# Performance work log

Measured on AMD Instinct MI355X. Metric: run time of the kernel, lower is better.

The kernel has to match this reference:

```python
import jax, jax.numpy as jnp
from jax import lax
import numpy as np

B, S, T = 1024, 512, 48


def setup_inputs() -> dict:
    key = jax.random.key(0)
    k1, k2, k3, k4, k5, k6 = jax.random.split(key, 6)
    emissions = jax.random.normal(k1, (B, S, T), dtype=jnp.float32)
    tags = jax.random.randint(k2, (B, S), 0, T, dtype=jnp.int32)
    # variable-length mask; length >= 1 so position 0 is always valid
    lengths = jax.random.randint(k3, (B,), 1, S + 1, dtype=jnp.int32)
    mask = (jnp.arange(S)[None, :] < lengths[:, None]).astype(jnp.float32)
    transitions = jax.random.normal(k4, (T, T), dtype=jnp.float32)
    start_transitions = jax.random.normal(k5, (T,), dtype=jnp.float32)
    end_transitions = jax.random.normal(k6, (T,), dtype=jnp.float32)
    return {
        "emissions": emissions,
        "tags": tags,
        "mask": mask,
        "transitions": transitions,
        "start_transitions": start_transitions,
        "end_transitions": end_transitions,
    }


def _gold_score(emissions, tags, mask, transitions, start_transitions, end_transitions):
    # score of the gold tag sequence (vectorized over time)
    score = start_transitions[tags[:, 0]]
    score = score + jnp.take_along_axis(emissions[:, 0], tags[:, 0:1], axis=1)[:, 0]
    # NOTE: original code indexes transitions[cur_tag, prev_tag] here (faithful)
    trans_sc = transitions[tags[:, 1:], tags[:, :-1]]                      # [B, S-1]
    emit_sc = jnp.take_along_axis(emissions[:, 1:], tags[:, 1:, None], axis=2)[..., 0]
    score = score + jnp.sum((trans_sc + emit_sc) * mask[:, 1:], axis=1)
    seq_last = mask.sum(axis=1).astype(jnp.int32) - 1                      # [B]
    last_tags = jnp.take_along_axis(tags, seq_last[:, None], axis=1)[:, 0]
    return score + end_transitions[last_tags]


def _forward_algorithm(emissions, mask, transitions, start_transitions, end_transitions):
    # log-partition via logsumexp recurrence, lax.scan over time
    init = start_transitions[None, :] + emissions[:, 0]                    # [B, T]

    def step(score, xs):
        em_i, m_i = xs                                                     # [B,T], [B]
        # next[b, cur] = logsumexp_prev(score[b,prev] + trans[prev,cur] + em[b,cur])
        ns = jax.nn.logsumexp(score[:, :, None] + transitions[None] + em_i[:, None, :], axis=1)
        score = jnp.where(m_i[:, None] > 0, ns, score)
        return score, None

    xs = (jnp.swapaxes(emissions[:, 1:], 0, 1), jnp.swapaxes(mask[:, 1:], 0, 1))
    score, _ = lax.scan(step, init, xs)
    return jax.nn.logsumexp(score + end_transitions[None, :], axis=1)      # [B]


def reference(emissions, tags, mask, transitions, start_transitions, end_transitions):
    gold = _gold_score(emissions, tags, mask, transitions, start_transitions, end_transitions)
    fwd = _forward_algorithm(emissions, mask, transitions, start_transitions, end_transitions)
    return (fwd - gold).mean()
```

## Files before the change

### kernel.cpp

```cpp
#include <hip/hip_runtime.h>


#define T 48
#define SLEN 512
#define BATCH 1024
#define STT (SLEN * T)
#define NB 16
#define LOG2E 1.4426950408889634f
#define LN2   0.6931471805599453f
#define ESC   6.0f

typedef float f4 __attribute__((ext_vector_type(4)));
typedef short s4 __attribute__((ext_vector_type(4)));

#if __has_builtin(__builtin_amdgcn_mfma_f32_16x16x16bf16_1k)
#define MFMA(a, b, c) __builtin_amdgcn_mfma_f32_16x16x16bf16_1k((a), (b), (c), 0, 0, 0)
#else
static __device__ __forceinline__ f4 MFMA(s4 a, s4 b, f4 c) {
    f4 d;
    asm volatile("v_mfma_f32_16x16x16_bf16 %0, %1, %2, %3"
                 : "=v"(d) : "v"(a), "v"(b), "v"(c));
    return d;
}
#endif

__device__ __forceinline__ float bpermf(int addr, float v) {
    return __int_as_float(__builtin_amdgcn_ds_bpermute(addr, __float_as_int(v)));
}
__device__ __forceinline__ unsigned bfpk(float x, float y) {
    return ((__float_as_uint(x) + 0x8000u) >> 16) |
           ((__float_as_uint(y) + 0x8000u) & 0xffff0000u);
}
__device__ __forceinline__ s4 pk4(f4 v) {
    union { unsigned u[2]; s4 s; } c;
    c.u[0] = bfpk(v.x, v.y); c.u[1] = bfpk(v.z, v.w);
    return c.s;
}
__device__ __forceinline__ f4 e4(f4 v) {
    f4 r;
    r.x = exp2f(v.x * LOG2E); r.y = exp2f(v.y * LOG2E);
    r.z = exp2f(v.z * LOG2E); r.w = exp2f(v.w * LOG2E);
    return r;
}
__device__ __forceinline__ s4 mkfrag(const float* tr, int base, int step) {
    f4 e;
    e.x = exp2f(tr[base] * LOG2E - ESC);
    e.y = exp2f(tr[base + step] * LOG2E - ESC);
    e.z = exp2f(tr[base + 2 * step] * LOG2E - ESC);
    e.w = exp2f(tr[base + 3 * step] * LOG2E - ESC);
    return pk4(e);
}

#define BL(K, lv, V) { K.x = lv ? V.x : K.x; K.y = lv ? V.y : K.y; \
                       K.z = lv ? V.z : K.z; K.w = lv ? V.w : K.w; }

#define RESC { \
    float mv = fmaxf(fmaxf(fmaxf(K0.x, K0.y), fmaxf(K0.z, K0.w)), \
                     fmaxf(fmaxf(K1.x, K1.y), fmaxf(K1.z, K1.w))); \
    mv = fmaxf(mv, fmaxf(fmaxf(K2.x, K2.y), fmaxf(K2.z, K2.w))); \
    mv = fmaxf(mv, bpermf(a16, mv)); mv = fmaxf(mv, bpermf(a32, mv)); \
    int e_ = ((__float_as_int(mv) >> 23) & 255) - 127; \
    e_ = e_ < -120 ? -120 : (e_ > 120 ? 120 : e_); \
    float sc_ = __int_as_float((127 - e_) << 23); \
    K0 *= sc_; K1 *= sc_; K2 *= sc_; L += (float)e_; }

#define MFMA9 \
    f4 c0 = {0.f, 0.f, 0.f, 0.f}, c1 = {0.f, 0.f, 0.f, 0.f}, c2 = {0.f, 0.f, 0.f, 0.f}; \
    c0 = MFMA(A00, B0, c0); c1 = MFMA(A10, B0, c1); c2 = MFMA(A20, B0, c2); \
    c0 = MFMA(A01, B1, c0); c1 = MFMA(A11, B1, c1); c2 = MFMA(A21, B1, c2); \
    c0 = MFMA(A02, B2, c0); c1 = MFMA(A12, B2, c1); c2 = MFMA(A22, B2, c2);

__global__ __launch_bounds__(192, 1) void crf_kernel(
    const float* __restrict__ em,
    const int*   __restrict__ tags,
    const float* __restrict__ mask,
    const float* __restrict__ tr,
    const float* __restrict__ start_t,
    const float* __restrict__ end_t,
    float*       __restrict__ out)
{
    const int tid  = threadIdx.x;
    const int wv   = tid >> 6;
    const int lane = tid & 63;
    const int l15  = lane & 15;
    const int q    = lane >> 4;
    const int bg   = blockIdx.x * NB;

    __shared__ float sP[NB * T];
    __shared__ float sLf[NB];
    __shared__ float sGold[NB];

    const int bb = lane >> 2, q3 = lane & 3;
    {
    }
    const f4* m4 = (const f4*)(mask + (size_t)(bg + bb) * SLEN + q3 * 128);
    float ms = 0.f;
    #pragma unroll 8
    for (int i = 0; i < 32; ++i) { f4 v = m4[i]; ms += (v.x + v.y) + (v.z + v.w); }
    ms += __shfl_xor(ms, 1); ms += __shfl_xor(ms, 2);
    const int len_team = (int)(ms + 0.5f);
    const int a16 = (lane ^ 16) << 2, a32 = (lane ^ 32) << 2;
    const int lenc = __builtin_amdgcn_ds_bpermute(l15 << 4, len_team);
    const int nf_c = (lenc - 1) >> 1;
    const int nb_c = (lenc - 1) - nf_c;

    if (wv == 2) {
        const int bi = bg + bb;
        const int*   tg = tags + (size_t)bi * SLEN;
        const float* eb = em + (size_t)bi * STT;
        float g0 = 0.f, g1 = 0.f;
        int i = 1 + q3;
        for (; i + 12 < len_team; i += 16) {
            int c0 = tg[i],      p0 = tg[i - 1];
            int c1 = tg[i + 4],  p1 = tg[i + 3];
            int c2 = tg[i + 8],  p2 = tg[i + 7];
            int c3 = tg[i + 12], p3 = tg[i + 11];
            g0 += tr[c0 * T + p0] + eb[i * T + c0];
            g1 += tr[c1 * T + p1] + eb[(i + 4) * T + c1];
            g0 += tr[c2 * T + p2] + eb[(i + 8) * T + c2];
            g1 += tr[c3 * T + p3] + eb[(i + 12) * T + c3];
        }
        for (; i < len_team; i += 4) {
            int c = tg[i], p = tg[i - 1];
            g0 += tr[c * T + p] + eb[i * T + c];
        }
        float g = g0 + g1;
        g += __shfl_xor(g, 1); g += __shfl_xor(g, 2);
        if (q3 == 0) {
            int t0 = tg[0], tl = tg[len_team - 1];
            sGold[bb] = g + start_t[t0] + eb[t0] + end_t[tl];
        }
    } else if (wv == 0) {
        s4 A00 = mkfrag(tr, (0  + 4*q) * T + 0  + l15, T);
        s4 A10 = mkfrag(tr, (0  + 4*q) * T + 16 + l15, T);
        s4 A20 = mkfrag(tr, (0  + 4*q) * T + 32 + l15, T);
        s4 A01 = mkfrag(tr, (16 + 4*q) * T + 0  + l15, T);
        s4 A11 = mkfrag(tr, (16 + 4*q) * T + 16 + l15, T);
        s4 A21 = mkfrag(tr, (16 + 4*q) * T + 32 + l15, T);
        s4 A02 = mkfrag(tr, (32 + 4*q) * T + 0  + l15, T);
        s4 A12 = mkfrag(tr, (32 + 4*q) * T + 16 + l15, T);
        s4 A22 = mkfrag(tr, (32 + 4*q) * T + 32 + l15, T);

        int mx = nf_c;
        mx = max(mx, __shfl_xor(mx, 1)); mx = max(mx, __shfl_xor(mx, 2));
        mx = max(mx, __shfl_xor(mx, 4)); mx = max(mx, __shfl_xor(mx, 8));

        const f4* p4b = (const f4*)(em + (size_t)(bg + l15) * STT);
        const f4* st4 = (const f4*)start_t;
        f4 K0, K1, K2;
        {
            f4 e0 = p4b[q], e1 = p4b[4 + q], e2 = p4b[8 + q];
            K0 = e4(e0 + st4[q]); K1 = e4(e1 + st4[4 + q]); K2 = e4(e2 + st4[8 + q]);
        }
        float L = 0.f;
        s4 B0 = pk4(K0), B1 = pk4(K1), B2 = pk4(K2);

        f4 R00,R01,R02, R10,R11,R12, R20,R21,R22, R30,R31,R32, W0,W1,W2;
        #define LDF(Sa,Sb,Sc, sidx) { int o_ = (sidx)*12 + q; Sa = p4b[o_]; Sb = p4b[o_+4]; Sc = p4b[o_+8]; }
        LDF(R00,R01,R02, 1) LDF(R10,R11,R12, 2) LDF(R20,R21,R22, 3) LDF(R30,R31,R32, 4)
        W0 = e4(R00); W1 = e4(R01); W2 = e4(R02);
        LDF(R00,R01,R02, 5)

        #define FIT(dd, Sa,Sb,Sc, RS) { \
            MFMA9 \
            bool lv = (dd) <= nf_c; \
            c0 = c0 * W0; c1 = c1 * W1; c2 = c2 * W2; \
            BL(K0, lv, c0) BL(K1, lv, c1) BL(K2, lv, c2) \
            if ((RS) && (((dd) & 7) == 0)) RESC \
            B0 = pk4(K0); B1 = pk4(K1); B2 = pk4(K2); \
            W0 = e4(Sa); W1 = e4(Sb); W2 = e4(Sc); \
            LDF(Sa,Sb,Sc, (dd) + 5) }

        int d = 1;
        for (; d + 3 <= mx; d += 4) {
            FIT(d,     R10,R11,R12, 0)
            FIT(d + 1, R20,R21,R22, 0)
            FIT(d + 2, R30,R31,R32, 0)
            FIT(d + 3, R00,R01,R02, 1)
        }
        if (d <= mx) { FIT(d, R10,R11,R12, 0)
            if (d + 1 <= mx) { FIT(d + 1, R20,R21,R22, 0)
                if (d + 2 <= mx) FIT(d + 2, R30,R31,R32, 0) } }
        #undef FIT
        #undef LDF

        f4* sp4 = (f4*)sP;
        int ob = l15 * 12 + q;
        sp4[ob] = K0; sp4[ob + 4] = K1; sp4[ob + 8] = K2;
        if (lane < 16) sLf[lane] = L + ESC * (float)nf_c;
    }

    float uK0x=0.f;
    if (wv == 1) {
        s4 A00 = mkfrag(tr, (0  + l15) * T + 0  + 4*q, 1);
        s4 A10 = mkfrag(tr, (16 + l15) * T + 0  + 4*q, 1);
        s4 A20 = mkfrag(tr, (32 + l15) * T + 0  + 4*q, 1);
        s4 A01 = mkfrag(tr, (0  + l15) * T + 16 + 4*q, 1);
        s4 A11 = mkfrag(tr, (16 + l15) * T + 16 + 4*q, 1);
        s4 A21 = mkfrag(tr, (32 + l15) * T + 16 + 4*q, 1);
        s4 A02 = mkfrag(tr, (0  + l15) * T + 32 + 4*q, 1);
        s4 A12 = mkfrag(tr, (16 + l15) * T + 32 + 4*q, 1);
        s4 A22 = mkfrag(tr, (32 + l15) * T + 32 + 4*q, 1);

        int mx = nb_c;
        mx = max(mx, __shfl_xor(mx, 1)); mx = max(mx, __shfl_xor(mx, 2));
        mx = max(mx, __shfl_xor(mx, 4)); mx = max(mx, __shfl_xor(mx, 8));

        const f4* p4b = (const f4*)(em + (size_t)(bg + l15) * STT);
        const f4* en4 = (const f4*)end_t;
        f4 K0 = e4(en4[q]), K1 = e4(en4[4 + q]), K2 = e4(en4[8 + q]);
        float L = 0.f;
        s4 B0, B1, B2;

        f4 R00,R01,R02, R10,R11,R12, R20,R21,R22, R30,R31,R32, W0,W1,W2;
        #define LDB(Sa,Sb,Sc, dd) { int sb_ = lenc - 1 - (dd); sb_ = sb_ < 0 ? 0 : sb_; \
            int o_ = sb_ * 12 + q; Sa = p4b[o_]; Sb = p4b[o_+4]; Sc = p4b[o_+8]; }
        LDB(R00,R01,R02, 0) LDB(R10,R11,R12, 1) LDB(R20,R21,R22, 2) LDB(R30,R31,R32, 3)
        W0 = e4(R00); W1 = e4(R01); W2 = e4(R02);
        LDB(R00,R01,R02, 4)

        #define BIT(dd, Sa,Sb,Sc, RS) { \
            f4 t0 = K0 * W0, t1 = K1 * W1, t2 = K2 * W2; \
            B0 = pk4(t0); B1 = pk4(t1); B2 = pk4(t2); \
            MFMA9 \
            bool lv = (dd) < nb_c; \
            BL(K0, lv, c0) BL(K1, lv, c1) BL(K2, lv, c2) \
            if ((RS) && (((dd) & 7) == 7)) RESC \
            W0 = e4(Sa); W1 = e4(Sb); W2 = e4(Sc); \
            LDB(Sa,Sb,Sc, (dd) + 5) }

        int d = 0;
        for (; d + 4 <= mx; d += 4) {
            BIT(d,     R10,R11,R12, 0)
            BIT(d + 1, R20,R21,R22, 0)
            BIT(d + 2, R30,R31,R32, 0)
            BIT(d + 3, R00,R01,R02, 1)
        }
        if (d < mx) { BIT(d, R10,R11,R12, 0)
            if (d + 1 < mx) { BIT(d + 1, R20,R21,R22, 0)
                if (d + 2 < mx) BIT(d + 2, R30,R31,R32, 0) } }
        #undef BIT
        #undef LDB

        __syncthreads();

        const f4* sp4 = (const f4*)sP;
        int ob = l15 * 12 + q;
        f4 p0 = sp4[ob], p1 = sp4[ob + 4], p2 = sp4[ob + 8];
        float part = p0.x * K0.x;
        part = fmaf(p0.y, K0.y, part); part = fmaf(p0.z, K0.z, part); part = fmaf(p0.w, K0.w, part);
        part = fmaf(p1.x, K1.x, part); part = fmaf(p1.y, K1.y, part);
        part = fmaf(p1.z, K1.z, part); part = fmaf(p1.w, K1.w, part);
        part = fmaf(p2.x, K2.x, part); part = fmaf(p2.y, K2.y, part);
        part = fmaf(p2.z, K2.z, part); part = fmaf(p2.w, K2.w, part);
        part += bpermf(a16, part); part += bpermf(a32, part);

        float res = 0.f;
        if (lane < 16) {
            float lz = (sLf[lane] + (L + ESC * (float)nb_c) + log2f(part)) * LN2;
            res = lz - sGold[lane];
        }
        #pragma unroll
        for (int m = 32; m >= 1; m >>= 1) res += __shfl_xor(res, m);
        if (lane == 0) atomicAdd(out, res * (1.0f / (float)BATCH));
    } else {
        __syncthreads();
    }
    (void)uK0x;
}

extern "C" void kernel_launch(void* const* d_in, const int* in_sizes, int n_in,
                              void* d_out, int out_size, void* d_ws, size_t ws_size,
                              hipStream_t stream) {
    const float* em      = (const float*)d_in[0];
    const int*   tags    = (const int*)  d_in[1];
    const float* mask    = (const float*)d_in[2];
    const float* trans   = (const float*)d_in[3];
    const float* start_t = (const float*)d_in[4];
    const float* end_t   = (const float*)d_in[5];
    float* out = (float*)d_out;

    hipMemsetAsync(out, 0, sizeof(float), stream);
    crf_kernel<<<BATCH / NB, 192, 0, stream>>>(em, tags, mask, trans, start_t, end_t, out);
}
```

Before: 230.2 us.

## Stage exp'd emissions through LDS with producer waves and split gold score blocks

Adds two producer waves that load emission chunks of 8 steps, exponentiate them, convert to fp16 and write them into double-buffered LDS. The forward and backward MFMA waves then read weights from LDS instead of issuing their own global loads and exps on the serial critical path. Gold-score computation moves to 64 extra blocks that atomically subtract their contribution, and the forward/backward split is swapped. In exchange, each chunk needs a block-wide barrier, fp16 storage loses precision on the exp'd emissions, and renormalisation now happens every chunk.

```diff
diff --git a/kernel.cpp b/kernel.cpp
--- a/kernel.cpp
+++ b/kernel.cpp
@@ -6,12 +6,17 @@
 #define BATCH 1024
 #define STT (SLEN * T)
 #define NB 16
+#define NBLK 64
+#define CH 8
+#define PADH 52
 #define LOG2E 1.4426950408889634f
 #define LN2   0.6931471805599453f
 #define ESC   6.0f
 
 typedef float f4 __attribute__((ext_vector_type(4)));
 typedef short s4 __attribute__((ext_vector_type(4)));
+typedef _Float16 h4v __attribute__((ext_vector_type(4)));
+typedef h4v h4 __attribute__((may_alias));
 
 #if __has_builtin(__builtin_amdgcn_mfma_f32_16x16x16bf16_1k)
 #define MFMA(a, b, c) __builtin_amdgcn_mfma_f32_16x16x16bf16_1k((a), (b), (c), 0, 0, 0)
@@ -42,6 +47,8 @@
     r.z = exp2f(v.z * LOG2E); r.w = exp2f(v.w * LOG2E);
     return r;
 }
+__device__ __forceinline__ h4 toh4(f4 v) { return __builtin_convertvector(v, h4v); }
+__device__ __forceinline__ f4 tof4(h4 h) { return __builtin_convertvector(h, f4); }
 __device__ __forceinline__ s4 mkfrag(const float* tr, int base, int step) {
     f4 e;
     e.x = exp2f(tr[base] * LOG2E - ESC);
@@ -65,12 +72,30 @@
     K0 *= sc_; K1 *= sc_; K2 *= sc_; L += (float)e_; }
 
 #define MFMA9 \
-    f4 c0 = {0.f, 0.f, 0.f, 0.f}, c1 = {0.f, 0.f, 0.f, 0.f}, c2 = {0.f, 0.f, 0.f, 0.f}; \
+    f4 c0 = {0.f,0.f,0.f,0.f}, c1 = {0.f,0.f,0.f,0.f}, c2 = {0.f,0.f,0.f,0.f}; \
     c0 = MFMA(A00, B0, c0); c1 = MFMA(A10, B0, c1); c2 = MFMA(A20, B0, c2); \
     c0 = MFMA(A01, B1, c0); c1 = MFMA(A11, B1, c1); c2 = MFMA(A21, B1, c2); \
     c0 = MFMA(A02, B2, c0); c1 = MFMA(A12, B2, c1); c2 = MFMA(A22, B2, c2);
 
-__global__ __launch_bounds__(192, 1) void crf_kernel(
+#define STAGE(c_, DIRIDX, SGEXPR) { \
+    f4 r_[24]; \
+    _Pragma("unroll") \
+    for (int s_ = 0; s_ < CH; ++s_) { \
+        int sg_ = (SGEXPR); \
+        sg_ = sg_ < 0 ? 0 : (sg_ > SLEN - 1 ? SLEN - 1 : sg_); \
+        const f4* src_ = (const f4*)(eb + (size_t)sg_ * T); \
+        r_[s_*3+0] = src_[p3*3+0]; r_[s_*3+1] = src_[p3*3+1]; r_[s_*3+2] = src_[p3*3+2]; \
+    } \
+    h4* dst_ = (h4*)sEm[DIRIDX][(c_) & 1]; \
+    _Pragma("unroll") \
+    for (int s_ = 0; s_ < CH; ++s_) { \
+        int o_ = (s_ * 16 + bat) * 13 + p3 * 3; \
+        dst_[o_+0] = toh4(e4(r_[s_*3+0])); \
+        dst_[o_+1] = toh4(e4(r_[s_*3+1])); \
+        dst_[o_+2] = toh4(e4(r_[s_*3+2])); \
+    } }
+
+__global__ __launch_bounds__(256, 1) void crf_kernel(
     const float* __restrict__ em,
     const int*   __restrict__ tags,
     const float* __restrict__ mask,
@@ -79,171 +104,156 @@
     const float* __restrict__ end_t,
     float*       __restrict__ out)
 {
-    const int tid  = threadIdx.x;
+    const int tid = threadIdx.x;
+
+    if (blockIdx.x >= NBLK) {
+        const int gb  = blockIdx.x - NBLK;
+        const int bat = tid >> 4, lq = tid & 15;
+        const int bi  = gb * NB + bat;
+        const float* mb = mask + (size_t)bi * SLEN;
+        const f4* m4 = (const f4*)mb;
+        float ms = 0.f;
+        #pragma unroll
+        for (int i = 0; i < 8; ++i) { f4 v = m4[lq * 8 + i]; ms += (v.x + v.y) + (v.z + v.w); }
+        ms += __shfl_xor(ms, 1); ms += __shfl_xor(ms, 2);
+        ms += __shfl_xor(ms, 4); ms += __shfl_xor(ms, 8);
+        const int len = (int)(ms + 0.5f);
+        const int*   tg = tags + (size_t)bi * SLEN;
+        const float* eb = em + (size_t)bi * STT;
+        float g = 0.f;
+        for (int i = 1 + lq; i < len; i += 16) {
+            int cc = tg[i], pp = tg[i - 1];
+            g += tr[cc * T + pp] + eb[(size_t)i * T + cc];
+        }
+        g += __shfl_xor(g, 1); g += __shfl_xor(g, 2);
+        g += __shfl_xor(g, 4); g += __shfl_xor(g, 8);
+        if (lq == 0) {
+            int t0 = tg[0], tl = tg[len - 1];
+            float gold = g + start_t[t0] + eb[t0] + end_t[tl];
+            atomicAdd(out, -gold * (1.0f / (float)BATCH));
+        }
+        return;
+    }
+
     const int wv   = tid >> 6;
     const int lane = tid & 63;
     const int l15  = lane & 15;
     const int q    = lane >> 4;
     const int bg   = blockIdx.x * NB;
 
+    __shared__ __align__(16) _Float16 sEm[2][2][CH * 16 * PADH];
     __shared__ float sP[NB * T];
     __shared__ float sLf[NB];
-    __shared__ float sGold[NB];
-
-    const int bb = lane >> 2, q3 = lane & 3;
-    {
-    }
-    const f4* m4 = (const f4*)(mask + (size_t)(bg + bb) * SLEN + q3 * 128);
+
+    const int bb = lane >> 2, p3 = lane & 3;
+    const f4* m4 = (const f4*)(mask + (size_t)(bg + bb) * SLEN + p3 * 128);
     float ms = 0.f;
     #pragma unroll 8
     for (int i = 0; i < 32; ++i) { f4 v = m4[i]; ms += (v.x + v.y) + (v.z + v.w); }
     ms += __shfl_xor(ms, 1); ms += __shfl_xor(ms, 2);
     const int len_team = (int)(ms + 0.5f);
+    const int lenc = __builtin_amdgcn_ds_bpermute(l15 << 4, len_team);
+    const int nf_c = (lenc - 1) - ((lenc - 1) >> 1);
+    const int nb_c = (lenc - 1) >> 1;
     const int a16 = (lane ^ 16) << 2, a32 = (lane ^ 32) << 2;
-    const int lenc = __builtin_amdgcn_ds_bpermute(l15 << 4, len_team);
-    const int nf_c = (lenc - 1) >> 1;
-    const int nb_c = (lenc - 1) - nf_c;
-
-    if (wv == 2) {
-        const int bi = bg + bb;
-        const int*   tg = tags + (size_t)bi * SLEN;
-        const float* eb = em + (size_t)bi * STT;
-        float g0 = 0.f, g1 = 0.f;
-        int i = 1 + q3;
-        for (; i + 12 < len_team; i += 16) {
-            int c0 = tg[i],      p0 = tg[i - 1];
-            int c1 = tg[i + 4],  p1 = tg[i + 3];
-            int c2 = tg[i + 8],  p2 = tg[i + 7];
-            int c3 = tg[i + 12], p3 = tg[i + 11];
-            g0 += tr[c0 * T + p0] + eb[i * T + c0];
-            g1 += tr[c1 * T + p1] + eb[(i + 4) * T + c1];
-            g0 += tr[c2 * T + p2] + eb[(i + 8) * T + c2];
-            g1 += tr[c3 * T + p3] + eb[(i + 12) * T + c3];
-        }
-        for (; i < len_team; i += 4) {
-            int c = tg[i], p = tg[i - 1];
-            g0 += tr[c * T + p] + eb[i * T + c];
-        }
-        float g = g0 + g1;
-        g += __shfl_xor(g, 1); g += __shfl_xor(g, 2);
-        if (q3 == 0) {
-            int t0 = tg[0], tl = tg[len_team - 1];
-            sGold[bb] = g + start_t[t0] + eb[t0] + end_t[tl];
-        }
-    } else if (wv == 0) {
-        s4 A00 = mkfrag(tr, (0  + 4*q) * T + 0  + l15, T);
-        s4 A10 = mkfrag(tr, (0  + 4*q) * T + 16 + l15, T);
-        s4 A20 = mkfrag(tr, (0  + 4*q) * T + 32 + l15, T);
-        s4 A01 = mkfrag(tr, (16 + 4*q) * T + 0  + l15, T);
-        s4 A11 = mkfrag(tr, (16 + 4*q) * T + 16 + l15, T);
-        s4 A21 = mkfrag(tr, (16 + 4*q) * T + 32 + l15, T);
-        s4 A02 = mkfrag(tr, (32 + 4*q) * T + 0  + l15, T);
-        s4 A12 = mkfrag(tr, (32 + 4*q) * T + 16 + l15, T);
-        s4 A22 = mkfrag(tr, (32 + 4*q) * T + 32 + l15, T);
-
-        int mx = nf_c;
-        mx = max(mx, __shfl_xor(mx, 1)); mx = max(mx, __shfl_xor(mx, 2));
-        mx = max(mx, __shfl_xor(mx, 4)); mx = max(mx, __shfl_xor(mx, 8));
-
+
+    int mxf = nf_c;
+    mxf = max(mxf, __shfl_xor(mxf, 1)); mxf = max(mxf, __shfl_xor(mxf, 2));
+    mxf = max(mxf, __shfl_xor(mxf, 4)); mxf = max(mxf, __shfl_xor(mxf, 8));
+    const int NCH = (mxf + 7) >> 3;
+
+    s4 A00{}, A10{}, A20{}, A01{}, A11{}, A21{}, A02{}, A12{}, A22{};
+    f4 K0{}, K1{}, K2{};
+    s4 B0{}, B1{}, B2{};
+    float L = 0.f;
+    const int bat = bb;
+    const float* eb = em + (size_t)(bg + bat) * STT;
+    const int lb = len_team;
+
+    if (wv == 0) {
+        A00 = mkfrag(tr, (0  + 4*q) * T + 0  + l15, T);
+        A10 = mkfrag(tr, (0  + 4*q) * T + 16 + l15, T);
+        A20 = mkfrag(tr, (0  + 4*q) * T + 32 + l15, T);
+        A01 = mkfrag(tr, (16 + 4*q) * T + 0  + l15, T);
+        A11 = mkfrag(tr, (16 + 4*q) * T + 16 + l15, T);
+        A21 = mkfrag(tr, (16 + 4*q) * T + 32 + l15, T);
+        A02 = mkfrag(tr, (32 + 4*q) * T + 0  + l15, T);
+        A12 = mkfrag(tr, (32 + 4*q) * T + 16 + l15, T);
+        A22 = mkfrag(tr, (32 + 4*q) * T + 32 + l15, T);
         const f4* p4b = (const f4*)(em + (size_t)(bg + l15) * STT);
         const f4* st4 = (const f4*)start_t;
-        f4 K0, K1, K2;
-        {
-            f4 e0 = p4b[q], e1 = p4b[4 + q], e2 = p4b[8 + q];
-            K0 = e4(e0 + st4[q]); K1 = e4(e1 + st4[4 + q]); K2 = e4(e2 + st4[8 + q]);
-        }
-        float L = 0.f;
-        s4 B0 = pk4(K0), B1 = pk4(K1), B2 = pk4(K2);
-
-        f4 R00,R01,R02, R10,R11,R12, R20,R21,R22, R30,R31,R32, W0,W1,W2;
-        #define LDF(Sa,Sb,Sc, sidx) { int o_ = (sidx)*12 + q; Sa = p4b[o_]; Sb = p4b[o_+4]; Sc = p4b[o_+8]; }
-        LDF(R00,R01,R02, 1) LDF(R10,R11,R12, 2) LDF(R20,R21,R22, 3) LDF(R30,R31,R32, 4)
-        W0 = e4(R00); W1 = e4(R01); W2 = e4(R02);
-        LDF(R00,R01,R02, 5)
-
-        #define FIT(dd, Sa,Sb,Sc, RS) { \
-            MFMA9 \
-            bool lv = (dd) <= nf_c; \
-            c0 = c0 * W0; c1 = c1 * W1; c2 = c2 * W2; \
-            BL(K0, lv, c0) BL(K1, lv, c1) BL(K2, lv, c2) \
-            if ((RS) && (((dd) & 7) == 0)) RESC \
-            B0 = pk4(K0); B1 = pk4(K1); B2 = pk4(K2); \
-            W0 = e4(Sa); W1 = e4(Sb); W2 = e4(Sc); \
-            LDF(Sa,Sb,Sc, (dd) + 5) }
-
-        int d = 1;
-        for (; d + 3 <= mx; d += 4) {
-            FIT(d,     R10,R11,R12, 0)
-            FIT(d + 1, R20,R21,R22, 0)
-            FIT(d + 2, R30,R31,R32, 0)
-            FIT(d + 3, R00,R01,R02, 1)
-        }
-        if (d <= mx) { FIT(d, R10,R11,R12, 0)
-            if (d + 1 <= mx) { FIT(d + 1, R20,R21,R22, 0)
-                if (d + 2 <= mx) FIT(d + 2, R30,R31,R32, 0) } }
-        #undef FIT
-        #undef LDF
-
+        K0 = e4(p4b[q] + st4[q]);
+        K1 = e4(p4b[4 + q] + st4[4 + q]);
+        K2 = e4(p4b[8 + q] + st4[8 + q]);
+        B0 = pk4(K0); B1 = pk4(K1); B2 = pk4(K2);
+    } else if (wv == 1) {
+        A00 = mkfrag(tr, (0  + l15) * T + 0  + 4*q, 1);
+        A10 = mkfrag(tr, (16 + l15) * T + 0  + 4*q, 1);
+        A20 = mkfrag(tr, (32 + l15) * T + 0  + 4*q, 1);
+        A01 = mkfrag(tr, (0  + l15) * T + 16 + 4*q, 1);
+        A11 = mkfrag(tr, (16 + l15) * T + 16 + 4*q, 1);
+        A21 = mkfrag(tr, (32 + l15) * T + 16 + 4*q, 1);
+        A02 = mkfrag(tr, (0  + l15) * T + 32 + 4*q, 1);
+        A12 = mkfrag(tr, (16 + l15) * T + 32 + 4*q, 1);
+        A22 = mkfrag(tr, (32 + l15) * T + 32 + 4*q, 1);
+        const f4* en4 = (const f4*)end_t;
+        K0 = e4(en4[q]); K1 = e4(en4[4 + q]); K2 = e4(en4[8 + q]);
+    } else if (wv == 2) {
+        STAGE(0, 0, 0 * CH + 1 + s_)
+    } else {
+        STAGE(0, 1, lb - 1 - (0 * CH + s_))
+    }
+
+    __syncthreads();
+
+    for (int c = 0; c < NCH; ++c) {
+        if (wv == 0) {
+            const h4* wb = ((const h4*)sEm[0][c & 1]) + l15 * 13 + q;
+            #pragma unroll
+            for (int s = 0; s < CH; ++s) {
+                f4 W0 = tof4(wb[s * 208 + 0]);
+                f4 W1 = tof4(wb[s * 208 + 4]);
+                f4 W2 = tof4(wb[s * 208 + 8]);
+                const int d = c * CH + 1 + s;
+                MFMA9
+                bool lv = d <= nf_c;
+                c0 = c0 * W0; c1 = c1 * W1; c2 = c2 * W2;
+                BL(K0, lv, c0) BL(K1, lv, c1) BL(K2, lv, c2)
+                if (s == CH - 1) RESC
+                B0 = pk4(K0); B1 = pk4(K1); B2 = pk4(K2);
+            }
+        } else if (wv == 1) {
+            const h4* wb = ((const h4*)sEm[1][c & 1]) + l15 * 13 + q;
+            #pragma unroll
+            for (int s = 0; s < CH; ++s) {
+                f4 W0 = tof4(wb[s * 208 + 0]);
+                f4 W1 = tof4(wb[s * 208 + 4]);
+                f4 W2 = tof4(wb[s * 208 + 8]);
+                f4 t0 = K0 * W0, t1 = K1 * W1, t2 = K2 * W2;
+                B0 = pk4(t0); B1 = pk4(t1); B2 = pk4(t2);
+                const int dd = c * CH + s;
+                MFMA9
+                bool lv = dd < nb_c;
+                BL(K0, lv, c0) BL(K1, lv, c1) BL(K2, lv, c2)
+                if (s == CH - 1) RESC
+            }
+        } else if (wv == 2) {
+            if (c + 1 < NCH) STAGE(c + 1, 0, (c + 1) * CH + 1 + s_)
+        } else {
+            if (c + 1 < NCH) STAGE(c + 1, 1, lb - 1 - ((c + 1) * CH + s_))
+        }
+        __syncthreads();
+    }
+
+    if (wv == 0) {
         f4* sp4 = (f4*)sP;
         int ob = l15 * 12 + q;
         sp4[ob] = K0; sp4[ob + 4] = K1; sp4[ob + 8] = K2;
         if (lane < 16) sLf[lane] = L + ESC * (float)nf_c;
     }
-
-    float uK0x=0.f;
+    __syncthreads();
+
     if (wv == 1) {
-        s4 A00 = mkfrag(tr, (0  + l15) * T + 0  + 4*q, 1);
-        s4 A10 = mkfrag(tr, (16 + l15) * T + 0  + 4*q, 1);
-        s4 A20 = mkfrag(tr, (32 + l15) * T + 0  + 4*q, 1);
-        s4 A01 = mkfrag(tr, (0  + l15) * T + 16 + 4*q, 1);
-        s4 A11 = mkfrag(tr, (16 + l15) * T + 16 + 4*q, 1);
-        s4 A21 = mkfrag(tr, (32 + l15) * T + 16 + 4*q, 1);
-        s4 A02 = mkfrag(tr, (0  + l15) * T + 32 + 4*q, 1);
-        s4 A12 = mkfrag(tr, (16 + l15) * T + 32 + 4*q, 1);
-        s4 A22 = mkfrag(tr, (32 + l15) * T + 32 + 4*q, 1);
-
-        int mx = nb_c;
-        mx = max(mx, __shfl_xor(mx, 1)); mx = max(mx, __shfl_xor(mx, 2));
-        mx = max(mx, __shfl_xor(mx, 4)); mx = max(mx, __shfl_xor(mx, 8));
-
-        const f4* p4b = (const f4*)(em + (size_t)(bg + l15) * STT);
-        const f4* en4 = (const f4*)end_t;
-        f4 K0 = e4(en4[q]), K1 = e4(en4[4 + q]), K2 = e4(en4[8 + q]);
-        float L = 0.f;
-        s4 B0, B1, B2;
-
-        f4 R00,R01,R02, R10,R11,R12, R20,R21,R22, R30,R31,R32, W0,W1,W2;
-        #define LDB(Sa,Sb,Sc, dd) { int sb_ = lenc - 1 - (dd); sb_ = sb_ < 0 ? 0 : sb_; \
-            int o_ = sb_ * 12 + q; Sa = p4b[o_]; Sb = p4b[o_+4]; Sc = p4b[o_+8]; }
-        LDB(R00,R01,R02, 0) LDB(R10,R11,R12, 1) LDB(R20,R21,R22, 2) LDB(R30,R31,R32, 3)
-        W0 = e4(R00); W1 = e4(R01); W2 = e4(R02);
-        LDB(R00,R01,R02, 4)
-
-        #define BIT(dd, Sa,Sb,Sc, RS) { \
-            f4 t0 = K0 * W0, t1 = K1 * W1, t2 = K2 * W2; \
-            B0 = pk4(t0); B1 = pk4(t1); B2 = pk4(t2); \
-            MFMA9 \
-            bool lv = (dd) < nb_c; \
-            BL(K0, lv, c0) BL(K1, lv, c1) BL(K2, lv, c2) \
-            if ((RS) && (((dd) & 7) == 7)) RESC \
-            W0 = e4(Sa); W1 = e4(Sb); W2 = e4(Sc); \
-            LDB(Sa,Sb,Sc, (dd) + 5) }
-
-        int d = 0;
-        for (; d + 4 <= mx; d += 4) {
-            BIT(d,     R10,R11,R12, 0)
-            BIT(d + 1, R20,R21,R22, 0)
-            BIT(d + 2, R30,R31,R32, 0)
-            BIT(d + 3, R00,R01,R02, 1)
-        }
-        if (d < mx) { BIT(d, R10,R11,R12, 0)
-            if (d + 1 < mx) { BIT(d + 1, R20,R21,R22, 0)
-                if (d + 2 < mx) BIT(d + 2, R30,R31,R32, 0) } }
-        #undef BIT
-        #undef LDB
-
-        __syncthreads();
-
         const f4* sp4 = (const f4*)sP;
         int ob = l15 * 12 + q;
         f4 p0 = sp4[ob], p1 = sp4[ob + 4], p2 = sp4[ob + 8];
@@ -258,15 +268,12 @@
         float res = 0.f;
         if (lane < 16) {
             float lz = (sLf[lane] + (L + ESC * (float)nb_c) + log2f(part)) * LN2;
-            res = lz - sGold[lane];
+            res = lz;
         }
         #pragma unroll
         for (int m = 32; m >= 1; m >>= 1) res += __shfl_xor(res, m);
         if (lane == 0) atomicAdd(out, res * (1.0f / (float)BATCH));
-    } else {
-        __syncthreads();
-    }
-    (void)uK0x;
+    }
 }
 
 extern "C" void kernel_launch(void* const* d_in, const int* in_sizes, int n_in,
@@ -281,5 +288,5 @@
     float* out = (float*)d_out;
 
     hipMemsetAsync(out, 0, sizeof(float), stream);
-    crf_kernel<<<BATCH / NB, 192, 0, stream>>>(em, tags, mask, trans, start_t, end_t, out);
-}
+    crf_kernel<<<NBLK + BATCH / NB, 256, 0, stream>>>(em, tags, mask, trans, start_t, end_t, out);
+}
```

Result: faster. 216.7 us (-5.9%).
